# Optimization experiments

Measured on AMD Instinct MI355X. Metric: run time of the kernel, lower is better.

The kernel has to match this reference:

```python
import jax, jax.numpy as jnp
import numpy as np

B, S, D = 2, 2048, 2048
H, HK = 16, 4          # n_heads, n_kv_heads
DK = D // H            # 128
REP = H // HK


def setup_inputs() -> dict:
    key = jax.random.key(0)
    ks = jax.random.split(key, 9)
    x = jax.random.normal(ks[0], (B, S, D), dtype=jnp.float32)
    # RoPE tables: [max_seq_len, d_k/2]
    inv_freq = 1.0 / (10000.0 ** (jnp.arange(0, DK, 2, dtype=jnp.float32) / DK))
    t = jnp.arange(S, dtype=jnp.float32)
    freqs = jnp.outer(t, inv_freq)  # [S, DK/2]
    freqs_cos = jnp.cos(freqs)
    freqs_sin = jnp.sin(freqs)
    sc = 0.02
    return {
        "x": x,
        "freqs_cos": freqs_cos,
        "freqs_sin": freqs_sin,
        "wq_w": jax.random.normal(ks[1], (D, D), dtype=jnp.float32) * sc,
        "wq_b": jnp.zeros((D,), dtype=jnp.float32),
        "wk_w": jax.random.normal(ks[2], (HK * DK, D), dtype=jnp.float32) * sc,
        "wk_b": jnp.zeros((HK * DK,), dtype=jnp.float32),
        "wv_w": jax.random.normal(ks[3], (HK * DK, D), dtype=jnp.float32) * sc,
        "wv_b": jnp.zeros((HK * DK,), dtype=jnp.float32),
        "wo_w": jax.random.normal(ks[4], (D, D), dtype=jnp.float32) * sc,
        "wo_b": jnp.zeros((D,), dtype=jnp.float32),
    }


def _apply_rope(t, cos, sin):
    # t: [b, h, s, dk]; cos/sin: [1, 1, s, dk/2]; interleaved pairs (even=real, odd=imag)
    tr = t[..., 0::2]
    ti = t[..., 1::2]
    out_r = tr * cos - ti * sin
    out_i = tr * sin + ti * cos
    return jnp.stack([out_r, out_i], axis=-1).reshape(t.shape)


def reference(x, freqs_cos, freqs_sin, wq_w, wq_b, wk_w, wk_b, wv_w, wv_b, wo_w, wo_b):
    b, s, d = x.shape
    q = (x @ wq_w.T + wq_b).reshape(b, s, H, DK).transpose(0, 2, 1, 3)   # [b,H,s,dk]
    k = (x @ wk_w.T + wk_b).reshape(b, s, HK, DK).transpose(0, 2, 1, 3)  # [b,HK,s,dk]
    v = (x @ wv_w.T + wv_b).reshape(b, s, HK, DK).transpose(0, 2, 1, 3)

    cos = freqs_cos[:s][None, None]  # [1,1,s,dk/2]
    sin = freqs_sin[:s][None, None]
    q = _apply_rope(q, cos, sin)
    k = _apply_rope(k, cos, sin)

    # GQA: group q heads by kv head instead of materializing repeat_kv
    qg = q.reshape(b, HK, REP, s, DK)
    scores = jnp.einsum("bgrqd,bgkd->bgrqk", qg, k) / jnp.sqrt(jnp.float32(DK))
    causal = jnp.triu(jnp.full((s, s), -jnp.inf, dtype=scores.dtype), k=1)
    attn = jax.nn.softmax(scores + causal, axis=-1)  # dropout=0.0 -> no-op
    out = jnp.einsum("bgrqk,bgkd->bgrqd", attn, v)   # [b,HK,REP,s,dk]
    out = out.reshape(b, H, s, DK).transpose(0, 2, 1, 3).reshape(b, s, d)
    return out @ wo_w.T + wo_b
```

## Files before the change

### kernel.cpp

```cpp
#include <hip/hip_runtime.h>

#define BDIM 2
#define SDIM 2048
#define DDIM 2048
#define HQ 16
#define HKV 4
#define DKH 128
#define NKV 512
#define NQKV 3072
#define MROWS 4096

typedef __attribute__((ext_vector_type(8))) short bf16x8;
typedef __attribute__((ext_vector_type(4))) float f32x4;
typedef __attribute__((ext_vector_type(8))) unsigned short u16x8;
typedef __attribute__((ext_vector_type(4))) unsigned short u16x4;

#define AS1 __attribute__((address_space(1)))
#define AS3 __attribute__((address_space(3)))

__device__ __forceinline__ unsigned short f2bf(float f) {
    union { float f; unsigned int u; } v; v.f = f;
    unsigned int r = v.u + 0x7FFFu + ((v.u >> 16) & 1u);
    return (unsigned short)(r >> 16);
}
__device__ __forceinline__ float bf2f(unsigned short u) {
    union { unsigned int u; float f; } v; v.u = ((unsigned int)u) << 16;
    return v.f;
}
__device__ __forceinline__ unsigned int pack2bf(float a, float b) {
    return (unsigned int)f2bf(a) | ((unsigned int)f2bf(b) << 16);
}

#define NX   ((size_t)MROWS * DDIM)
#define NWQ  ((size_t)DDIM * DDIM)
#define NWKV ((size_t)NKV * DDIM)
__global__ void cast_all(const float* __restrict__ x, const float* __restrict__ wq,
                         const float* __restrict__ wk, const float* __restrict__ wv,
                         const float* __restrict__ wo, unsigned short* __restrict__ dst) {
    size_t i = ((size_t)blockIdx.x * blockDim.x + threadIdx.x) * 4;
    const size_t N0 = NX, N1 = N0 + NWQ, N2 = N1 + NWKV, N3 = N2 + NWKV, N4 = N3 + NWQ;
    if (i >= N4) return;
    const float* src; size_t off;
    if (i < N0)      { src = x;  off = i; }
    else if (i < N1) { src = wq; off = i - N0; }
    else if (i < N2) { src = wk; off = i - N1; }
    else if (i < N3) { src = wv; off = i - N2; }
    else             { src = wo; off = i - N3; }
    float4 v = *(const float4*)(src + off);
    u16x4 o;
    o[0] = f2bf(v.x); o[1] = f2bf(v.y); o[2] = f2bf(v.z); o[3] = f2bf(v.w);
    *(u16x4*)(dst + i) = o;
}

__global__ void concat_bias(const float* __restrict__ qb, const float* __restrict__ kb,
                            const float* __restrict__ vb, float* __restrict__ o) {
    int i = blockIdx.x * blockDim.x + threadIdx.x;
    if (i < DDIM) o[i] = qb[i];
    else if (i < DDIM + NKV) o[i] = kb[i - DDIM];
    else if (i < NQKV) o[i] = vb[i - DDIM - NKV];
}

__global__ void rope_v(unsigned short* __restrict__ buf,
                       const float* __restrict__ cosT, const float* __restrict__ sinT,
                       float qscale) {
    int r = blockIdx.x, pos = r & (SDIM - 1);
    int col0 = threadIdx.x * 8;
    unsigned short* p = buf + (size_t)r * NQKV + col0;
    int i0 = (col0 & 127) >> 1;
    float4 c4 = *(const float4*)(cosT + pos * 64 + i0);
    float4 s4 = *(const float4*)(sinT + pos * 64 + i0);
    float sc = (col0 < DDIM) ? qscale : 1.f;
    u16x8 v = *(const u16x8*)p;
    u16x8 o;
    float cc[4] = {c4.x, c4.y, c4.z, c4.w}, ss[4] = {s4.x, s4.y, s4.z, s4.w};
#pragma unroll
    for (int k = 0; k < 4; ++k) {
        float xr = bf2f(v[2 * k]), xi = bf2f(v[2 * k + 1]);
        o[2 * k]     = f2bf((xr * cc[k] - xi * ss[k]) * sc);
        o[2 * k + 1] = f2bf((xr * ss[k] + xi * cc[k]) * sc);
    }
    *(u16x8*)p = o;
}

__global__ void transpose_v(const unsigned short* __restrict__ qkv,
                            unsigned short* __restrict__ Vt) {
    __shared__ unsigned short T[32][33];
    int s0 = blockIdx.x * 32, d0 = blockIdx.y * 32, b = blockIdx.z;
    int c = threadIdx.x & 31, r4 = threadIdx.x >> 5;
    for (int rr = r4; rr < 32; rr += 8)
        T[rr][c] = qkv[(size_t)(b * SDIM + s0 + rr) * NQKV + (DDIM + NKV) + d0 + c];
    __syncthreads();
    int cp = ((c & 0x0C) << 1) | ((c & 0x10) >> 2) | (c & 3);
    for (int rr = r4; rr < 32; rr += 8)
        Vt[(size_t)(b * NKV + d0 + rr) * SDIM + s0 + cp] = T[c][rr];
}

template <int BF16OUT>
__global__ __launch_bounds__(256) void gemm_bt(
    const unsigned short* __restrict__ A,
    const unsigned short* __restrict__ Bm,
    const float* __restrict__ bias,
    void* __restrict__ Cv,
    int pitch, int Kdim) {
    __shared__ unsigned short As[128 * 32];
    __shared__ unsigned short Bs[128 * 32];
    const int tid = threadIdx.x;
    const int w = tid >> 6, lane = tid & 63;
    const int ml = lane & 15, quad = lane >> 4;
    const int m0 = blockIdx.y * 128, n0 = blockIdx.x * 128;
    const int wr = (w >> 1) * 64, wc = (w & 1) * 64;

    f32x4 acc[4][4] = {};

    const int c0 = tid, c1 = tid + 256;
    const int ar0 = c0 >> 2, ak0 = (c0 & 3) * 8;
    const int ar1 = c1 >> 2, ak1 = (c1 & 3) * 8;

    for (int kt = 0; kt < Kdim; kt += 32) {
        __builtin_amdgcn_global_load_lds(
            (const AS1 unsigned int*)(A + (size_t)(m0 + ar0) * Kdim + kt + ak0),
            (AS3 unsigned int*)(As + c0 * 8), 16, 0, 0);
        __builtin_amdgcn_global_load_lds(
            (const AS1 unsigned int*)(A + (size_t)(m0 + ar1) * Kdim + kt + ak1),
            (AS3 unsigned int*)(As + c1 * 8), 16, 0, 0);
        __builtin_amdgcn_global_load_lds(
            (const AS1 unsigned int*)(Bm + (size_t)(n0 + ar0) * Kdim + kt + ak0),
            (AS3 unsigned int*)(Bs + c0 * 8), 16, 0, 0);
        __builtin_amdgcn_global_load_lds(
            (const AS1 unsigned int*)(Bm + (size_t)(n0 + ar1) * Kdim + kt + ak1),
            (AS3 unsigned int*)(Bs + c1 * 8), 16, 0, 0);
        __syncthreads();

        bf16x8 af[4], bfr[4];
#pragma unroll
        for (int i = 0; i < 4; ++i)
            af[i] = *(const bf16x8*)&As[(wr + i * 16 + ml) * 32 + quad * 8];
#pragma unroll
        for (int j = 0; j < 4; ++j)
            bfr[j] = *(const bf16x8*)&Bs[(wc + j * 16 + ml) * 32 + quad * 8];
#pragma unroll
        for (int i = 0; i < 4; ++i)
#pragma unroll
            for (int j = 0; j < 4; ++j)
                acc[i][j] = __builtin_amdgcn_mfma_f32_16x16x32_bf16(af[i], bfr[j], acc[i][j], 0, 0, 0);
        __syncthreads();
    }

#pragma unroll
    for (int j = 0; j < 4; ++j) {
        int col = n0 + wc + j * 16 + ml;
        float bj = bias[col];
#pragma unroll
        for (int i = 0; i < 4; ++i) {
            int row0 = m0 + wr + i * 16 + quad * 4;
#pragma unroll
            for (int r = 0; r < 4; ++r) {
                float v = acc[i][j][r] + bj;
                if (BF16OUT)
                    ((unsigned short*)Cv)[(size_t)(row0 + r) * pitch + col] = f2bf(v);
                else
                    ((float*)Cv)[(size_t)(row0 + r) * pitch + col] = v;
            }
        }
    }
}

__global__ __launch_bounds__(256, 2) void attn_fwd(
    const unsigned short* __restrict__ Qp,
    const unsigned short* __restrict__ Kp,
    const unsigned short* __restrict__ Vt,
    unsigned short* __restrict__ O) {
    const int l = blockIdx.x;
    const int j = l >> 5;
    const int h = l & 15;
    const int b = (l >> 4) & 1;
    const int g = h >> 2;
    const int tid = threadIdx.x;
    const int w = tid >> 6, lane = tid & 63;
    const int ml = lane & 15, quad = lane >> 4;
    const int seg = lane & 3, rsub = lane >> 2;

    __shared__ unsigned short Ks[4 * 64 * 32];
    __shared__ unsigned short Vs[2 * 128 * 32];

    const bool low_pair = ((w < 2) != (l & 1));
    const int myqt = low_pair ? j : (31 - j);
    const int q0 = myqt * 64 + (w & 1) * 32;
    const int ktend = 32 - j;

    bf16x8 aq[2][4];
#pragma unroll
    for (int g2 = 0; g2 < 2; ++g2) {
        const size_t qrow = (size_t)(b * SDIM + q0 + g2 * 16 + ml);
#pragma unroll
        for (int kc = 0; kc < 4; ++kc)
            aq[g2][kc] = *(const bf16x8*)(Qp + qrow * NQKV + h * DKH + kc * 32 + quad * 8);
    }

    f32x4 o_acc[2][8] = {};
    float m_run[2] = {-INFINITY, -INFINITY}, l_run[2] = {0.f, 0.f};

    for (int kt = 0; kt < ktend; ++kt) {
        const int kb = kt * 64;
        __syncthreads();
#pragma unroll
        for (int kc = 0; kc < 4; ++kc)
            __builtin_amdgcn_global_load_lds(
                (const AS1 unsigned int*)(Kp + (size_t)(b * SDIM + kb + w * 16 + rsub) * NQKV + g * DKH + kc * 32 + seg * 8),
                (AS3 unsigned int*)(Ks + kc * 2048 + w * 512 + lane * 8), 16, 0, 0);
#pragma unroll
        for (int c = 0; c < 4; ++c) {
            int u = w * 4 + c, kc2 = u >> 3, rg = u & 7;
            __builtin_amdgcn_global_load_lds(
                (const AS1 unsigned int*)(Vt + (size_t)(b * NKV + g * DKH + rg * 16 + rsub) * SDIM + kb + kc2 * 32 + seg * 8),
                (AS3 unsigned int*)(Vs + u * 512 + lane * 8), 16, 0, 0);
        }
        __syncthreads();

        if (kb <= q0 + 31) {
            f32x4 st[2][4];
#pragma unroll
            for (int t = 0; t < 4; ++t) {
                bf16x8 ak[4];
#pragma unroll
                for (int kc = 0; kc < 4; ++kc)
                    ak[kc] = *(const bf16x8*)&Ks[kc * 2048 + (t * 16 + ml) * 32 + quad * 8];
#pragma unroll
                for (int g2 = 0; g2 < 2; ++g2) {
                    f32x4 sc = {};
#pragma unroll
                    for (int kc = 0; kc < 4; ++kc)
                        sc = __builtin_amdgcn_mfma_f32_16x16x32_bf16(ak[kc], aq[g2][kc], sc, 0, 0, 0);
                    st[g2][t] = sc;
                }
            }

            const bool diag = (kb + 63 > q0);
            float mx[2] = {-INFINITY, -INFINITY};
            if (diag) {
#pragma unroll
                for (int g2 = 0; g2 < 2; ++g2) {
                    int qg = q0 + g2 * 16 + ml;
#pragma unroll
                    for (int t = 0; t < 4; ++t) {
                        int kvb = kb + t * 16 + quad * 4;
#pragma unroll
                        for (int r = 0; r < 4; ++r) {
                            float x = st[g2][t][r];
                            if (kvb + r > qg) x = -INFINITY;
                            st[g2][t][r] = x;
                            mx[g2] = fmaxf(mx[g2], x);
                        }
                    }
                }
            } else {
#pragma unroll
                for (int g2 = 0; g2 < 2; ++g2)
#pragma unroll
                    for (int t = 0; t < 4; ++t)
#pragma unroll
                        for (int r = 0; r < 4; ++r)
                            mx[g2] = fmaxf(mx[g2], st[g2][t][r]);
            }

            float alpha[2];
            unsigned int pk[2][4][2];
            bool resc = false;
#pragma unroll
            for (int g2 = 0; g2 < 2; ++g2) {
                float m = mx[g2];
                m = fmaxf(m, __shfl_xor(m, 16));
                m = fmaxf(m, __shfl_xor(m, 32));
                float m_new = fmaxf(m_run[g2], m);
                resc = resc || (m_new > m_run[g2]);
                alpha[g2] = __expf(m_run[g2] - m_new);
                m_run[g2] = m_new;

                float lad = 0.f;
#pragma unroll
                for (int t = 0; t < 4; ++t) {
                    float p0 = __expf(st[g2][t][0] - m_new);
                    float p1 = __expf(st[g2][t][1] - m_new);
                    float p2 = __expf(st[g2][t][2] - m_new);
                    float p3 = __expf(st[g2][t][3] - m_new);
                    lad += (p0 + p1) + (p2 + p3);
                    pk[g2][t][0] = pack2bf(p0, p1);
                    pk[g2][t][1] = pack2bf(p2, p3);
                }
                lad += __shfl_xor(lad, 16);
                lad += __shfl_xor(lad, 32);
                l_run[g2] = l_run[g2] * alpha[g2] + lad;
            }

            if (__ballot(resc)) {
#pragma unroll
                for (int g2 = 0; g2 < 2; ++g2)
#pragma unroll
                    for (int dt = 0; dt < 8; ++dt)
#pragma unroll
                        for (int r = 0; r < 4; ++r)
                            o_acc[g2][dt][r] *= alpha[g2];
            }

#pragma unroll
            for (int c = 0; c < 2; ++c) {
                union { unsigned int u[4]; bf16x8 v; } pb[2];
#pragma unroll
                for (int g2 = 0; g2 < 2; ++g2) {
                    pb[g2].u[0] = pk[g2][2 * c][0];     pb[g2].u[1] = pk[g2][2 * c][1];
                    pb[g2].u[2] = pk[g2][2 * c + 1][0]; pb[g2].u[3] = pk[g2][2 * c + 1][1];
                }
#pragma unroll
                for (int dt = 0; dt < 8; ++dt) {
                    bf16x8 av = *(const bf16x8*)&Vs[c * 4096 + (dt * 16 + ml) * 32 + quad * 8];
                    o_acc[0][dt] = __builtin_amdgcn_mfma_f32_16x16x32_bf16(av, pb[0].v, o_acc[0][dt], 0, 0, 0);
                    o_acc[1][dt] = __builtin_amdgcn_mfma_f32_16x16x32_bf16(av, pb[1].v, o_acc[1][dt], 0, 0, 0);
                }
            }
        }
    }

#pragma unroll
    for (int g2 = 0; g2 < 2; ++g2) {
        float inv = 1.f / l_run[g2];
        size_t rowbase = (size_t)(b * SDIM + q0 + g2 * 16 + ml) * DDIM + h * DKH + quad * 4;
#pragma unroll
        for (int dt = 0; dt < 8; ++dt) {
            u16x4 ov;
#pragma unroll
            for (int r = 0; r < 4; ++r)
                ov[r] = f2bf(o_acc[g2][dt][r] * inv);
            *(u16x4*)(O + rowbase + dt * 16) = ov;
        }
    }
}

extern "C" void kernel_launch(void* const* d_in, const int* in_sizes, int n_in,
                              void* d_out, int out_size, void* d_ws, size_t ws_size,
                              hipStream_t stream) {
    const float* x    = (const float*)d_in[0];
    const float* fcos = (const float*)d_in[1];
    const float* fsin = (const float*)d_in[2];
    const float* wq_w = (const float*)d_in[3];
    const float* wq_b = (const float*)d_in[4];
    const float* wk_w = (const float*)d_in[5];
    const float* wk_b = (const float*)d_in[6];
    const float* wv_w = (const float*)d_in[7];
    const float* wv_b = (const float*)d_in[8];
    const float* wo_w = (const float*)d_in[9];
    const float* wo_b = (const float*)d_in[10];
    float* out = (float*)d_out;

    char* ws = (char*)d_ws;
    size_t off = 0;
    auto alloc = [&](size_t bytes) {
        char* p = ws + off;
        off += (bytes + 255) & ~(size_t)255;
        return p;
    };
    unsigned short* xb  = (unsigned short*)alloc(NX * 2);
    unsigned short* W3  = (unsigned short*)alloc((size_t)NQKV * DDIM * 2);
    unsigned short* wob = (unsigned short*)alloc(NWQ * 2);
    float* b3           = (float*)alloc((size_t)NQKV * 4);
    unsigned short* qkv = (unsigned short*)alloc((size_t)MROWS * NQKV * 2);
    unsigned short* Vt  = (unsigned short*)alloc((size_t)BDIM * NKV * SDIM * 2);
    unsigned short* att = (unsigned short*)alloc((size_t)MROWS * DDIM * 2);

    const size_t total4 = (NX + 2 * NWQ + 2 * NWKV) / 4;
    cast_all<<<dim3((unsigned)((total4 + 255) / 256)), dim3(256), 0, stream>>>(x, wq_w, wk_w, wv_w, wo_w, xb);
    concat_bias<<<dim3(12), dim3(256), 0, stream>>>(wq_b, wk_b, wv_b, b3);

    gemm_bt<1><<<dim3(NQKV / 128, MROWS / 128), 256, 0, stream>>>(xb, W3, b3, qkv, NQKV, DDIM);

    const float scale = 0.08838834764831845f;
    rope_v<<<dim3(MROWS), dim3(320), 0, stream>>>(qkv, fcos, fsin, scale);
    transpose_v<<<dim3(SDIM / 32, NKV / 32, BDIM), 256, 0, stream>>>(qkv, Vt);

    attn_fwd<<<dim3(512), dim3(256), 0, stream>>>(qkv, qkv + DDIM, Vt, att);

    gemm_bt<0><<<dim3(DDIM / 128, MROWS / 128), 256, 0, stream>>>(att, wob, wo_b, out, DDIM, DDIM);
}
```

Before: 334.3 us.

## Swizzle LDS tiles to avoid bank conflicts and fuse small prep kernels

Applies an XOR swizzle to the global-to-LDS load offsets and matching LDS read offsets in the GEMM and attention kernels, so fragment reads spread across LDS banks. Also folds the bias concatenation into the cast kernel and merges RoPE with the V transpose into one launch, removing two kernel launches. The swizzle must be consistent between the A and B operands, which it is because it depends only on the row within 16-row groups.

```diff
diff --git a/kernel.cpp b/kernel.cpp
--- a/kernel.cpp
+++ b/kernel.cpp
@@ -34,12 +34,21 @@
 #define NX   ((size_t)MROWS * DDIM)
 #define NWQ  ((size_t)DDIM * DDIM)
 #define NWKV ((size_t)NKV * DDIM)
+#define CAST_BLOCKS 18432
 __global__ void cast_all(const float* __restrict__ x, const float* __restrict__ wq,
                          const float* __restrict__ wk, const float* __restrict__ wv,
-                         const float* __restrict__ wo, unsigned short* __restrict__ dst) {
+                         const float* __restrict__ wo, unsigned short* __restrict__ dst,
+                         const float* __restrict__ qb, const float* __restrict__ kb,
+                         const float* __restrict__ vb, float* __restrict__ b3) {
+    if (blockIdx.x >= CAST_BLOCKS) {
+        int i = (blockIdx.x - CAST_BLOCKS) * 256 + threadIdx.x;
+        if (i < DDIM) b3[i] = qb[i];
+        else if (i < DDIM + NKV) b3[i] = kb[i - DDIM];
+        else if (i < NQKV) b3[i] = vb[i - DDIM - NKV];
+        return;
+    }
     size_t i = ((size_t)blockIdx.x * blockDim.x + threadIdx.x) * 4;
-    const size_t N0 = NX, N1 = N0 + NWQ, N2 = N1 + NWKV, N3 = N2 + NWKV, N4 = N3 + NWQ;
-    if (i >= N4) return;
+    const size_t N0 = NX, N1 = N0 + NWQ, N2 = N1 + NWKV, N3 = N2 + NWKV;
     const float* src; size_t off;
     if (i < N0)      { src = x;  off = i; }
     else if (i < N1) { src = wq; off = i - N0; }
@@ -52,47 +61,40 @@
     *(u16x4*)(dst + i) = o;
 }
 
-__global__ void concat_bias(const float* __restrict__ qb, const float* __restrict__ kb,
-                            const float* __restrict__ vb, float* __restrict__ o) {
-    int i = blockIdx.x * blockDim.x + threadIdx.x;
-    if (i < DDIM) o[i] = qb[i];
-    else if (i < DDIM + NKV) o[i] = kb[i - DDIM];
-    else if (i < NQKV) o[i] = vb[i - DDIM - NKV];
-}
-
-__global__ void rope_v(unsigned short* __restrict__ buf,
-                       const float* __restrict__ cosT, const float* __restrict__ sinT,
-                       float qscale) {
-    int r = blockIdx.x, pos = r & (SDIM - 1);
-    int col0 = threadIdx.x * 8;
-    unsigned short* p = buf + (size_t)r * NQKV + col0;
-    int i0 = (col0 & 127) >> 1;
-    float4 c4 = *(const float4*)(cosT + pos * 64 + i0);
-    float4 s4 = *(const float4*)(sinT + pos * 64 + i0);
-    float sc = (col0 < DDIM) ? qscale : 1.f;
-    u16x8 v = *(const u16x8*)p;
-    u16x8 o;
-    float cc[4] = {c4.x, c4.y, c4.z, c4.w}, ss[4] = {s4.x, s4.y, s4.z, s4.w};
-#pragma unroll
-    for (int k = 0; k < 4; ++k) {
-        float xr = bf2f(v[2 * k]), xi = bf2f(v[2 * k + 1]);
-        o[2 * k]     = f2bf((xr * cc[k] - xi * ss[k]) * sc);
-        o[2 * k + 1] = f2bf((xr * ss[k] + xi * cc[k]) * sc);
-    }
-    *(u16x8*)p = o;
-}
-
-__global__ void transpose_v(const unsigned short* __restrict__ qkv,
-                            unsigned short* __restrict__ Vt) {
-    __shared__ unsigned short T[32][33];
-    int s0 = blockIdx.x * 32, d0 = blockIdx.y * 32, b = blockIdx.z;
-    int c = threadIdx.x & 31, r4 = threadIdx.x >> 5;
-    for (int rr = r4; rr < 32; rr += 8)
-        T[rr][c] = qkv[(size_t)(b * SDIM + s0 + rr) * NQKV + (DDIM + NKV) + d0 + c];
-    __syncthreads();
-    int cp = ((c & 0x0C) << 1) | ((c & 0x10) >> 2) | (c & 3);
-    for (int rr = r4; rr < 32; rr += 8)
-        Vt[(size_t)(b * NKV + d0 + rr) * SDIM + s0 + cp] = T[c][rr];
+__global__ void rope_trans(unsigned short* __restrict__ buf,
+                           const float* __restrict__ cosT, const float* __restrict__ sinT,
+                           unsigned short* __restrict__ Vt, float qscale) {
+    if (blockIdx.x < MROWS) {
+        int r = blockIdx.x, pos = r & (SDIM - 1);
+        int col0 = threadIdx.x * 8;
+        unsigned short* p = buf + (size_t)r * NQKV + col0;
+        int i0 = (col0 & 127) >> 1;
+        float4 c4 = *(const float4*)(cosT + pos * 64 + i0);
+        float4 s4 = *(const float4*)(sinT + pos * 64 + i0);
+        float sc = (col0 < DDIM) ? qscale : 1.f;
+        u16x8 v = *(const u16x8*)p;
+        u16x8 o;
+        float cc[4] = {c4.x, c4.y, c4.z, c4.w}, ss[4] = {s4.x, s4.y, s4.z, s4.w};
+#pragma unroll
+        for (int k = 0; k < 4; ++k) {
+            float xr = bf2f(v[2 * k]), xi = bf2f(v[2 * k + 1]);
+            o[2 * k]     = f2bf((xr * cc[k] - xi * ss[k]) * sc);
+            o[2 * k + 1] = f2bf((xr * ss[k] + xi * cc[k]) * sc);
+        }
+        *(u16x8*)p = o;
+    } else {
+        __shared__ unsigned short T[32][33];
+        if (threadIdx.x >= 256) return;
+        int t = blockIdx.x - MROWS;
+        int s0 = (t & 63) * 32, d0 = ((t >> 6) & 15) * 32, b = t >> 10;
+        int c = threadIdx.x & 31, r4 = threadIdx.x >> 5;
+        for (int rr = r4; rr < 32; rr += 8)
+            T[rr][c] = buf[(size_t)(b * SDIM + s0 + rr) * NQKV + (DDIM + NKV) + d0 + c];
+        __syncthreads();
+        int cp = ((c & 0x0C) << 1) | ((c & 0x10) >> 2) | (c & 3);
+        for (int rr = r4; rr < 32; rr += 8)
+            Vt[(size_t)(b * NKV + d0 + rr) * SDIM + s0 + cp] = T[c][rr];
+    }
 }
 
 template <int BF16OUT>
@@ -109,12 +111,14 @@
     const int ml = lane & 15, quad = lane >> 4;
     const int m0 = blockIdx.y * 128, n0 = blockIdx.x * 128;
     const int wr = (w >> 1) * 64, wc = (w & 1) * 64;
+    const int swz = ((quad ^ (ml & 3) ^ ((ml >> 2) & 3))) * 8;
 
     f32x4 acc[4][4] = {};
 
     const int c0 = tid, c1 = tid + 256;
-    const int ar0 = c0 >> 2, ak0 = (c0 & 3) * 8;
-    const int ar1 = c1 >> 2, ak1 = (c1 & 3) * 8;
+    const int ar0 = c0 >> 2, ar1 = c1 >> 2;
+    const int ak0 = ((c0 & 3) ^ ((c0 >> 2) & 3) ^ ((c0 >> 4) & 3)) * 8;
+    const int ak1 = ((c1 & 3) ^ ((c1 >> 2) & 3) ^ ((c1 >> 4) & 3)) * 8;
 
     for (int kt = 0; kt < Kdim; kt += 32) {
         __builtin_amdgcn_global_load_lds(
@@ -134,10 +138,10 @@
         bf16x8 af[4], bfr[4];
 #pragma unroll
         for (int i = 0; i < 4; ++i)
-            af[i] = *(const bf16x8*)&As[(wr + i * 16 + ml) * 32 + quad * 8];
+            af[i] = *(const bf16x8*)&As[(wr + i * 16 + ml) * 32 + swz];
 #pragma unroll
         for (int j = 0; j < 4; ++j)
-            bfr[j] = *(const bf16x8*)&Bs[(wc + j * 16 + ml) * 32 + quad * 8];
+            bfr[j] = *(const bf16x8*)&Bs[(wc + j * 16 + ml) * 32 + swz];
 #pragma unroll
         for (int i = 0; i < 4; ++i)
 #pragma unroll
@@ -178,7 +182,9 @@
     const int tid = threadIdx.x;
     const int w = tid >> 6, lane = tid & 63;
     const int ml = lane & 15, quad = lane >> 4;
-    const int seg = lane & 3, rsub = lane >> 2;
+    const int rsub = lane >> 2;
+    const int segsw = ((lane & 3) ^ ((lane >> 2) & 3) ^ ((lane >> 4) & 3));
+    const int swz = ((quad ^ (ml & 3) ^ ((ml >> 2) & 3))) * 8;
 
     __shared__ unsigned short Ks[4 * 64 * 32];
     __shared__ unsigned short Vs[2 * 128 * 32];
@@ -206,13 +212,13 @@
 #pragma unroll
         for (int kc = 0; kc < 4; ++kc)
             __builtin_amdgcn_global_load_lds(
-                (const AS1 unsigned int*)(Kp + (size_t)(b * SDIM + kb + w * 16 + rsub) * NQKV + g * DKH + kc * 32 + seg * 8),
+                (const AS1 unsigned int*)(Kp + (size_t)(b * SDIM + kb + w * 16 + rsub) * NQKV + g * DKH + kc * 32 + segsw * 8),
                 (AS3 unsigned int*)(Ks + kc * 2048 + w * 512 + lane * 8), 16, 0, 0);
 #pragma unroll
         for (int c = 0; c < 4; ++c) {
             int u = w * 4 + c, kc2 = u >> 3, rg = u & 7;
             __builtin_amdgcn_global_load_lds(
-                (const AS1 unsigned int*)(Vt + (size_t)(b * NKV + g * DKH + rg * 16 + rsub) * SDIM + kb + kc2 * 32 + seg * 8),
+                (const AS1 unsigned int*)(Vt + (size_t)(b * NKV + g * DKH + rg * 16 + rsub) * SDIM + kb + kc2 * 32 + segsw * 8),
                 (AS3 unsigned int*)(Vs + u * 512 + lane * 8), 16, 0, 0);
         }
         __syncthreads();
@@ -224,7 +230,7 @@
                 bf16x8 ak[4];
 #pragma unroll
                 for (int kc = 0; kc < 4; ++kc)
-                    ak[kc] = *(const bf16x8*)&Ks[kc * 2048 + (t * 16 + ml) * 32 + quad * 8];
+                    ak[kc] = *(const bf16x8*)&Ks[kc * 2048 + (t * 16 + ml) * 32 + swz];
 #pragma unroll
                 for (int g2 = 0; g2 < 2; ++g2) {
                     f32x4 sc = {};
@@ -312,7 +318,7 @@
                 }
 #pragma unroll
                 for (int dt = 0; dt < 8; ++dt) {
-                    bf16x8 av = *(const bf16x8*)&Vs[c * 4096 + (dt * 16 + ml) * 32 + quad * 8];
+                    bf16x8 av = *(const bf16x8*)&Vs[c * 4096 + (dt * 16 + ml) * 32 + swz];
                     o_acc[0][dt] = __builtin_amdgcn_mfma_f32_16x16x32_bf16(av, pb[0].v, o_acc[0][dt], 0, 0, 0);
                     o_acc[1][dt] = __builtin_amdgcn_mfma_f32_16x16x32_bf16(av, pb[1].v, o_acc[1][dt], 0, 0, 0);
                 }
@@ -366,15 +372,13 @@
     unsigned short* Vt  = (unsigned short*)alloc((size_t)BDIM * NKV * SDIM * 2);
     unsigned short* att = (unsigned short*)alloc((size_t)MROWS * DDIM * 2);
 
-    const size_t total4 = (NX + 2 * NWQ + 2 * NWKV) / 4;
-    cast_all<<<dim3((unsigned)((total4 + 255) / 256)), dim3(256), 0, stream>>>(x, wq_w, wk_w, wv_w, wo_w, xb);
-    concat_bias<<<dim3(12), dim3(256), 0, stream>>>(wq_b, wk_b, wv_b, b3);
+    cast_all<<<dim3(CAST_BLOCKS + 12), dim3(256), 0, stream>>>(
+        x, wq_w, wk_w, wv_w, wo_w, xb, wq_b, wk_b, wv_b, b3);
 
     gemm_bt<1><<<dim3(NQKV / 128, MROWS / 128), 256, 0, stream>>>(xb, W3, b3, qkv, NQKV, DDIM);
 
     const float scale = 0.08838834764831845f;
-    rope_v<<<dim3(MROWS), dim3(320), 0, stream>>>(qkv, fcos, fsin, scale);
-    transpose_v<<<dim3(SDIM / 32, NKV / 32, BDIM), 256, 0, stream>>>(qkv, Vt);
+    rope_trans<<<dim3(MROWS + 2048), dim3(320), 0, stream>>>(qkv, fcos, fsin, Vt, scale);
 
     attn_fwd<<<dim3(512), dim3(256), 0, stream>>>(qkv, qkv + DDIM, Vt, att);
 
```

After: 332.5 us. About the same (-0.5%).
